# Kernel optimization log

Measured on AMD Instinct MI355X. Metric: run time of the kernel, lower is better.

Reference implementation:

```python
import jax, jax.numpy as jnp
import numpy as np


def _sig_gram(X, Y, n):
    """Signature-kernel gram matrix via the Goursat PDE recurrence.
    X: (A, M, D), Y: (B, N, D). Returns (A, B) of k(x_a, y_b).
    Recurrence: K[i+1,j+1] = K[i+1,j] + K[i,j+1] + K[i,j]*(inc_ij - 1).
    """
    f = 2 ** n
    # dyadic refinement: increments scaled by 1/2^n, each repeated 2^n times
    dX = jnp.repeat((X[:, 1:] - X[:, :-1]) / f, f, axis=1)  # (A, Mg-1, D)
    dY = jnp.repeat((Y[:, 1:] - Y[:, :-1]) / f, f, axis=1)  # (B, Ng-1, D)
    inc = jnp.einsum('aid,bjd->abij', dX, dY)               # (A, B, Mg-1, Ng-1)
    A, B, _, Ng1 = inc.shape
    ones_col = jnp.ones((A, B, 1), inc.dtype)

    def row_step(K_prev, inc_row):
        # K_prev: row i of the PDE grid, shape (A,B,Ng1+1); inc_row: (A,B,Ng1)
        diag = K_prev[..., :-1] * (inc_row - 1.0)  # K[i,j]*inc - K[i,j]
        up = K_prev[..., 1:]                        # K[i,j+1]

        def col_step(k_left, uv):
            u, d = uv
            k = k_left + u + d
            return k, k

        _, krow = jax.lax.scan(
            col_step,
            jnp.ones((A, B), inc.dtype),
            (jnp.moveaxis(up, -1, 0), jnp.moveaxis(diag, -1, 0)),
        )
        K_new = jnp.concatenate([ones_col, jnp.moveaxis(krow, 0, -1)], axis=-1)
        return K_new, None

    K0 = jnp.ones((A, B, Ng1 + 1), inc.dtype)  # boundary row K[0,:] = 1
    K_last, _ = jax.lax.scan(row_step, K0, jnp.moveaxis(inc, 2, 0))
    return K_last[..., -1]  # K[-1,-1] for every pair


def setup_inputs() -> dict:
    key = jax.random.key(0)
    kx, ky = jax.random.split(key)
    SCALE = 0.05  # keep kernel values in fp32 range (exponential growth)
    X = jax.random.normal(kx, (64, 128, 16), dtype=jnp.float32) * SCALE
    Y = jax.random.normal(ky, (64, 128, 16), dtype=jnp.float32) * SCALE
    return {"X": X, "Y": Y, "n": 0}


def reference(X, Y, n):
    k_xx = _sig_gram(X, X, n)
    k_yy = _sig_gram(Y, Y, n)
    k_xy = _sig_gram(X, Y, n)
    return jnp.mean(k_xx) + jnp.mean(k_yy) - 2.0 * jnp.mean(k_xy)
```

## Files before the change

kernel.cpp:

```cpp
#include <hip/hip_runtime.h>


#define XY_BLOCKS 1024
#define TRI_BLOCKS 544
#define NBLOCKS (XY_BLOCKS + 2 * TRI_BLOCKS)
#define DINC_PER 130048
#define WS_OUT_OFF (2 * DINC_PER)
#define NOUT (NBLOCKS * 4)

template <int C, int RM, int BM, bool BC>
__device__ __forceinline__ float dpp0(float x) {
    return __builtin_bit_cast(float, __builtin_amdgcn_update_dpp(
        0, __builtin_bit_cast(int, x), C, RM, BM, BC));
}

__device__ __forceinline__ float wave_scan_incl(float v) {
    v += dpp0<0x111, 0xf, 0xf, true>(v);
    v += dpp0<0x112, 0xf, 0xf, true>(v);
    v += dpp0<0x114, 0xf, 0xf, true>(v);
    v += dpp0<0x118, 0xf, 0xf, true>(v);
    v += dpp0<0x142, 0xa, 0xf, false>(v);
    v += dpp0<0x143, 0xc, 0xf, false>(v);
    return v;
}

__device__ __forceinline__ float wave_shr1(float x, float oldv) {
    return __builtin_bit_cast(float, __builtin_amdgcn_update_dpp(
        __builtin_bit_cast(int, oldv), __builtin_bit_cast(int, x),
        0x138, 0xf, 0xf, false));
}

__global__ __launch_bounds__(256) void sig_diff(
    const float* __restrict__ X, const float* __restrict__ Y,
    float* __restrict__ dInc)
{
    int i = blockIdx.x * 256 + threadIdx.x;
    if (i >= 65024) return;
    int which = (i >= 32512) ? 1 : 0;
    int j = i - which * 32512;
    int a = j / 508;
    int rq = j - a * 508;
    const float* S = which ? Y : X;
    const float4* p = (const float4*)(S + a * 2048) + rq;
    float4 v0 = p[0], v1 = p[4];
    float4 d;
    d.x = v1.x - v0.x; d.y = v1.y - v0.y;
    d.z = v1.z - v0.z; d.w = v1.w - v0.w;
    ((float4*)dInc)[i] = d;
}

__global__ __launch_bounds__(256) void sig_pde2(
    const float* __restrict__ dInc, float* __restrict__ outw)
{
    const int B = blockIdx.x;
    const int w = threadIdx.x >> 6, lane = threadIdx.x & 63;

    int g, a, b0;
    if (B < XY_BLOCKS) {
        g = 2; a = B >> 4; b0 = (B & 15) << 2;
    } else {
        int t = B - XY_BLOCKS; g = 0;
        if (t >= TRI_BLOCKS) { t -= TRI_BLOCKS; g = 1; }
        int aa = 0;
        for (;;) { int nb = (67 - aa) >> 2; if (t < nb) break; t -= nb; ++aa; }
        a = aa; b0 = aa + (t << 2);
    }
    const int b = b0 + w;
    const int slot = (B << 2) + w;
    if (g < 2 && b > 63) { if (lane == 0) outw[slot] = 0.0f; return; }

    const float* dXb = dInc;
    const float* dYb = dInc + DINC_PER;
    const float* dA = (g == 1) ? dYb : dXb;
    const float* dB = (g == 0) ? dXb : dYb;
    const float weight = (g == 2) ? (-2.0f / 4096.0f)
                                  : ((a == b ? 1.0f : 2.0f) / 4096.0f);

    float ya[16], yb_[16];
    {
        const float* Qb = dB + b * 2032;
        const int j0 = lane << 1;
        const int j1 = (j0 + 1 < 127) ? j0 + 1 : 126;
        const float4* A4 = (const float4*)(Qb + j0 * 16);
        const float4* B4 = (const float4*)(Qb + j1 * 16);
#pragma unroll
        for (int q = 0; q < 4; ++q) {
            float4 va = A4[q], vb = B4[q];
            ya[4*q+0] = va.x; ya[4*q+1] = va.y; ya[4*q+2] = va.z; ya[4*q+3] = va.w;
            yb_[4*q+0] = vb.x; yb_[4*q+1] = vb.y; yb_[4*q+2] = vb.z; yb_[4*q+3] = vb.w;
        }
    }

    const int abase = __builtin_amdgcn_readfirstlane(a * 2032);
    const float4* Ar = (const float4*)(dA + abase);

    float xr[16], xn[16];
#pragma unroll
    for (int q = 0; q < 4; ++q) {
        float4 v = Ar[q];
        xr[4*q+0] = v.x; xr[4*q+1] = v.y; xr[4*q+2] = v.z; xr[4*q+3] = v.w;
    }

    float g_lo = 1.0f, g_hi = 1.0f;
    const bool last = (lane == 63);

    for (int r = 0; r < 127; ++r) {
        const int rn = (r < 126) ? r + 1 : 126;
#pragma unroll
        for (int q = 0; q < 4; ++q) {
            float4 v = Ar[4 * rn + q];
            xn[4*q+0] = v.x; xn[4*q+1] = v.y; xn[4*q+2] = v.z; xn[4*q+3] = v.w;
        }
        float s0 = -0.5f, s1 = -0.5f, t0 = -0.5f, t1 = -0.5f;
#pragma unroll
        for (int d = 0; d < 16; d += 2) {
            s0 = fmaf(xr[d], ya[d], s0);    s1 = fmaf(xr[d+1], ya[d+1], s1);
            t0 = fmaf(xr[d], yb_[d], t0);   t1 = fmaf(xr[d+1], yb_[d+1], t1);
        }
        const float i0 = s0 + s1;
        const float i1 = t0 + t1;

        const float gl = wave_shr1(g_hi, 1.0f);
        const float c0 = fmaf(gl, i0, g_lo);
        const float c1 = last ? 0.0f : fmaf(g_lo, i1, g_hi);
        const float S = wave_scan_incl(c0 + c1);
        g_lo = (S - c1) + 1.0f;
        g_hi = S + 1.0f;
#pragma unroll
        for (int d = 0; d < 16; ++d) xr[d] = xn[d];
    }

    const float kab = __builtin_bit_cast(float,
        __builtin_amdgcn_readlane(__builtin_bit_cast(int, g_lo), 63));
    if (lane == 0) outw[slot] = weight * kab;
}

__global__ __launch_bounds__(256) void sig_reduce2(
    const float* __restrict__ v, float* __restrict__ out, int n)
{
    __shared__ float red[256];
    float s = 0.0f;
    for (int i = threadIdx.x; i < n; i += 256) s += v[i];
    red[threadIdx.x] = s;
    __syncthreads();
    for (int st = 128; st > 0; st >>= 1) {
        if (threadIdx.x < st) red[threadIdx.x] += red[threadIdx.x + st];
        __syncthreads();
    }
    if (threadIdx.x == 0) out[0] = red[0];
}

__global__ __launch_bounds__(64) void sig_pde_kernel(
    const float* __restrict__ X, const float* __restrict__ Y,
    float* __restrict__ ws)
{
    __shared__ float Xs[2048];
    const int T = blockIdx.x;
    const int g = T >> 12;
    const int t = T & 4095;
    const int a = t >> 6, b = t & 63;
    const int lane = threadIdx.x;
    if (g < 2 && a > b) { if (lane == 0) ws[T] = 0.0f; return; }
    const float* P = (g == 1) ? Y : X;
    const float* Q = (g == 0) ? X : Y;
    const float weight = (g == 2) ? (-2.0f / 4096.0f)
                                  : ((a == b ? 1.0f : 2.0f) / 4096.0f);
    {
        const float4* Pa = (const float4*)(P + a * 2048);
        float4* Xs4 = (float4*)Xs;
#pragma unroll
        for (int k = 0; k < 8; ++k) Xs4[lane + (k << 6)] = Pa[lane + (k << 6)];
    }
    __syncthreads();
    {
        float tmp[32];
#pragma unroll
        for (int k = 0; k < 32; ++k) {
            int idx = lane + (k << 6);
            tmp[k] = (idx < 2032) ? (Xs[idx + 16] - Xs[idx]) : 0.0f;
        }
        __syncthreads();
#pragma unroll
        for (int k = 0; k < 32; ++k) {
            int idx = lane + (k << 6);
            if (idx < 2032) Xs[idx] = tmp[k];
        }
    }
    __syncthreads();
    float y0[16], y1[16];
    {
        const float* Qb = Q + b * 2048;
        const int r0 = lane << 1;
        const int r2 = (r0 + 2 > 127) ? 127 : (r0 + 2);
        const float4* A4 = (const float4*)(Qb + r0 * 16);
        const float4* B4 = (const float4*)(Qb + (r0 + 1) * 16);
        const float4* C4 = (const float4*)(Qb + r2 * 16);
#pragma unroll
        for (int q = 0; q < 4; ++q) {
            float4 ra = A4[q], rb = B4[q], rc = C4[q];
            y0[4*q+0] = rb.x - ra.x;  y1[4*q+0] = rc.x - rb.x;
            y0[4*q+1] = rb.y - ra.y;  y1[4*q+1] = rc.y - rb.y;
            y0[4*q+2] = rb.z - ra.z;  y1[4*q+2] = rc.z - rb.z;
            y0[4*q+3] = rb.w - ra.w;  y1[4*q+3] = rc.w - rb.w;
        }
    }
    float g_lo = 1.0f, g_hi = 1.0f;
    const bool last = (lane == 63);
    for (int r = 0; r < 127; ++r) {
        const float* xrow = Xs + r * 16;
        float s0 = -0.5f, s1 = -0.5f, t0 = -0.5f, t1 = -0.5f;
#pragma unroll
        for (int d = 0; d < 16; d += 2) {
            s0 = fmaf(xrow[d], y0[d], s0);   s1 = fmaf(xrow[d+1], y0[d+1], s1);
            t0 = fmaf(xrow[d], y1[d], t0);   t1 = fmaf(xrow[d+1], y1[d+1], t1);
        }
        const float i0 = s0 + s1, i1 = t0 + t1;
        const float gl = wave_shr1(g_hi, 1.0f);
        const float c0 = fmaf(gl, i0, g_lo);
        const float c1 = last ? 0.0f : fmaf(g_lo, i1, g_hi);
        const float S = wave_scan_incl(c0 + c1);
        g_lo = (S - c1) + 1.0f;
        g_hi = S + 1.0f;
    }
    const float kab = __builtin_bit_cast(float,
        __builtin_amdgcn_readlane(__builtin_bit_cast(int, g_lo), 63));
    if (lane == 0) ws[T] = weight * kab;
}

extern "C" void kernel_launch(void* const* d_in, const int* in_sizes, int n_in,
                              void* d_out, int out_size, void* d_ws, size_t ws_size,
                              hipStream_t stream) {
    const float* X = (const float*)d_in[0];
    const float* Y = (const float*)d_in[1];
    float* out = (float*)d_out;
    float* ws  = (float*)d_ws;

    const size_t need = (size_t)(WS_OUT_OFF + NOUT) * sizeof(float);
    if (ws_size >= need) {
        sig_diff<<<254, 256, 0, stream>>>(X, Y, ws);
        sig_pde2<<<NBLOCKS, 256, 0, stream>>>(ws, ws + WS_OUT_OFF);
        sig_reduce2<<<1, 256, 0, stream>>>(ws + WS_OUT_OFF, out, NOUT);
    } else {
        sig_pde_kernel<<<12288, 64, 0, stream>>>(X, Y, ws);
        sig_reduce2<<<1, 256, 0, stream>>>(ws, out, 12288);
    }
}
```

Baseline: 149.4 us.

## Process two pairs per wave to interleave scans and fuse reduction via atomics

Each wave now computes the PDE for two (a,b) pairs that share the same x row, so the two independent DPP scan chains can interleave and hide each other's latency, and each loaded x row is reused twice. The triangular pair enumeration is changed to pack pairs in twos, which reduces wasted padded waves. The separate reduction kernel is removed: blocks sum their results in shared memory and atomically add into the output, which sig_diff zeroes first. This saves one kernel launch, but the fp32 atomic summation order becomes nondeterministic and each wave holds more registers.

```diff
diff --git a/kernel.cpp b/kernel.cpp
--- a/kernel.cpp
+++ b/kernel.cpp
@@ -1,12 +1,9 @@
 #include <hip/hip_runtime.h>
 
 
-#define XY_BLOCKS 1024
-#define TRI_BLOCKS 544
-#define NBLOCKS (XY_BLOCKS + 2 * TRI_BLOCKS)
 #define DINC_PER 130048
-#define WS_OUT_OFF (2 * DINC_PER)
-#define NOUT (NBLOCKS * 4)
+#define NDUO 4160
+#define NBLOCKS (NDUO / 4)
 
 template <int C, int RM, int BM, bool BC>
 __device__ __forceinline__ float dpp0(float x) {
@@ -30,10 +27,39 @@
         0x138, 0xf, 0xf, false));
 }
 
+__device__ __forceinline__ void pde_row(
+    const float* xr, const float* ya, const float* yb,
+    float& g_lo, float& g_hi, int lane)
+{
+    float s0 = -0.5f, s1 = -0.5f, t0 = -0.5f, t1 = -0.5f;
+#pragma unroll
+    for (int d = 0; d < 16; d += 2) {
+        s0 = fmaf(xr[d], ya[d], s0);    s1 = fmaf(xr[d+1], ya[d+1], s1);
+        t0 = fmaf(xr[d], yb[d], t0);    t1 = fmaf(xr[d+1], yb[d+1], t1);
+    }
+    const float i0 = s0 + s1;
+    const float i1 = t0 + t1;
+    const float gl = wave_shr1(g_hi, 1.0f);
+    const float c0 = fmaf(gl, i0, g_lo);
+    const float c1 = (lane == 63) ? 0.0f : fmaf(g_lo, i1, g_hi);
+    const float S = wave_scan_incl(c0 + c1);
+    g_lo = (S - c1) + 1.0f;
+    g_hi = S + 1.0f;
+}
+
+__device__ __forceinline__ void load_xrow(float* x, const float4* Ar, int r) {
+#pragma unroll
+    for (int q = 0; q < 4; ++q) {
+        float4 v = Ar[4 * r + q];
+        x[4*q+0] = v.x; x[4*q+1] = v.y; x[4*q+2] = v.z; x[4*q+3] = v.w;
+    }
+}
+
 __global__ __launch_bounds__(256) void sig_diff(
     const float* __restrict__ X, const float* __restrict__ Y,
-    float* __restrict__ dInc)
-{
+    float* __restrict__ dInc, float* __restrict__ outp)
+{
+    if (blockIdx.x == 0 && threadIdx.x == 0) outp[0] = 0.0f;
     int i = blockIdx.x * 256 + threadIdx.x;
     if (i >= 65024) return;
     int which = (i >= 32512) ? 1 : 0;
@@ -49,105 +75,79 @@
     ((float4*)dInc)[i] = d;
 }
 
-__global__ __launch_bounds__(256) void sig_pde2(
-    const float* __restrict__ dInc, float* __restrict__ outw)
-{
-    const int B = blockIdx.x;
-    const int w = threadIdx.x >> 6, lane = threadIdx.x & 63;
-
-    int g, a, b0;
-    if (B < XY_BLOCKS) {
-        g = 2; a = B >> 4; b0 = (B & 15) << 2;
+__global__ __launch_bounds__(256) void sig_pde3(
+    const float* __restrict__ dInc, float* __restrict__ outp)
+{
+    __shared__ float red[4];
+    const int wv = threadIdx.x >> 6, lane = threadIdx.x & 63;
+    const int T = (blockIdx.x << 2) + wv;
+
+    int g, a, b1, b2;
+    float w1, w2;
+    if (T < 2048) {
+        g = 2; a = T >> 5;
+        b1 = (T & 31) << 1; b2 = b1 + 1;
+        w1 = w2 = -2.0f / 4096.0f;
     } else {
-        int t = B - XY_BLOCKS; g = 0;
-        if (t >= TRI_BLOCKS) { t -= TRI_BLOCKS; g = 1; }
+        int t = T - 2048;
+        g = (t >= 1056) ? 1 : 0;
+        if (g) t -= 1056;
         int aa = 0;
-        for (;;) { int nb = (67 - aa) >> 2; if (t < nb) break; t -= nb; ++aa; }
-        a = aa; b0 = aa + (t << 2);
-    }
-    const int b = b0 + w;
-    const int slot = (B << 2) + w;
-    if (g < 2 && b > 63) { if (lane == 0) outw[slot] = 0.0f; return; }
-
-    const float* dXb = dInc;
-    const float* dYb = dInc + DINC_PER;
-    const float* dA = (g == 1) ? dYb : dXb;
-    const float* dB = (g == 0) ? dXb : dYb;
-    const float weight = (g == 2) ? (-2.0f / 4096.0f)
-                                  : ((a == b ? 1.0f : 2.0f) / 4096.0f);
-
-    float ya[16], yb_[16];
-    {
-        const float* Qb = dB + b * 2032;
+        for (;;) { int nd = (65 - aa) >> 1; if (t < nd) break; t -= nd; ++aa; }
+        a = aa; b1 = a + (t << 1); b2 = b1 + 1;
+        w1 = (b1 == a ? 1.0f : 2.0f) / 4096.0f;
+        w2 = (b2 <= 63) ? (2.0f / 4096.0f) : 0.0f;
+        if (b2 > 63) b2 = 63;
+    }
+
+    const float* dA = (g == 1) ? (dInc + DINC_PER) : dInc;
+    const float* dB = (g == 0) ? dInc : (dInc + DINC_PER);
+
+    float yaA[16], ybA[16], yaB[16], ybB[16];
+    {
         const int j0 = lane << 1;
         const int j1 = (j0 + 1 < 127) ? j0 + 1 : 126;
-        const float4* A4 = (const float4*)(Qb + j0 * 16);
-        const float4* B4 = (const float4*)(Qb + j1 * 16);
+        const float4* A4 = (const float4*)(dB + b1 * 2032 + j0 * 16);
+        const float4* B4 = (const float4*)(dB + b1 * 2032 + j1 * 16);
+        const float4* C4 = (const float4*)(dB + b2 * 2032 + j0 * 16);
+        const float4* D4 = (const float4*)(dB + b2 * 2032 + j1 * 16);
 #pragma unroll
         for (int q = 0; q < 4; ++q) {
-            float4 va = A4[q], vb = B4[q];
-            ya[4*q+0] = va.x; ya[4*q+1] = va.y; ya[4*q+2] = va.z; ya[4*q+3] = va.w;
-            yb_[4*q+0] = vb.x; yb_[4*q+1] = vb.y; yb_[4*q+2] = vb.z; yb_[4*q+3] = vb.w;
+            float4 va = A4[q], vb = B4[q], vc = C4[q], vd = D4[q];
+            yaA[4*q+0]=va.x; yaA[4*q+1]=va.y; yaA[4*q+2]=va.z; yaA[4*q+3]=va.w;
+            ybA[4*q+0]=vb.x; ybA[4*q+1]=vb.y; ybA[4*q+2]=vb.z; ybA[4*q+3]=vb.w;
+            yaB[4*q+0]=vc.x; yaB[4*q+1]=vc.y; yaB[4*q+2]=vc.z; yaB[4*q+3]=vc.w;
+            ybB[4*q+0]=vd.x; ybB[4*q+1]=vd.y; ybB[4*q+2]=vd.z; ybB[4*q+3]=vd.w;
         }
     }
 
     const int abase = __builtin_amdgcn_readfirstlane(a * 2032);
     const float4* Ar = (const float4*)(dA + abase);
 
-    float xr[16], xn[16];
-#pragma unroll
-    for (int q = 0; q < 4; ++q) {
-        float4 v = Ar[q];
-        xr[4*q+0] = v.x; xr[4*q+1] = v.y; xr[4*q+2] = v.z; xr[4*q+3] = v.w;
-    }
-
-    float g_lo = 1.0f, g_hi = 1.0f;
-    const bool last = (lane == 63);
-
-    for (int r = 0; r < 127; ++r) {
-        const int rn = (r < 126) ? r + 1 : 126;
-#pragma unroll
-        for (int q = 0; q < 4; ++q) {
-            float4 v = Ar[4 * rn + q];
-            xn[4*q+0] = v.x; xn[4*q+1] = v.y; xn[4*q+2] = v.z; xn[4*q+3] = v.w;
-        }
-        float s0 = -0.5f, s1 = -0.5f, t0 = -0.5f, t1 = -0.5f;
-#pragma unroll
-        for (int d = 0; d < 16; d += 2) {
-            s0 = fmaf(xr[d], ya[d], s0);    s1 = fmaf(xr[d+1], ya[d+1], s1);
-            t0 = fmaf(xr[d], yb_[d], t0);   t1 = fmaf(xr[d+1], yb_[d+1], t1);
-        }
-        const float i0 = s0 + s1;
-        const float i1 = t0 + t1;
-
-        const float gl = wave_shr1(g_hi, 1.0f);
-        const float c0 = fmaf(gl, i0, g_lo);
-        const float c1 = last ? 0.0f : fmaf(g_lo, i1, g_hi);
-        const float S = wave_scan_incl(c0 + c1);
-        g_lo = (S - c1) + 1.0f;
-        g_hi = S + 1.0f;
-#pragma unroll
-        for (int d = 0; d < 16; ++d) xr[d] = xn[d];
-    }
-
-    const float kab = __builtin_bit_cast(float,
-        __builtin_amdgcn_readlane(__builtin_bit_cast(int, g_lo), 63));
-    if (lane == 0) outw[slot] = weight * kab;
-}
-
-__global__ __launch_bounds__(256) void sig_reduce2(
-    const float* __restrict__ v, float* __restrict__ out, int n)
-{
-    __shared__ float red[256];
-    float s = 0.0f;
-    for (int i = threadIdx.x; i < n; i += 256) s += v[i];
-    red[threadIdx.x] = s;
-    __syncthreads();
-    for (int st = 128; st > 0; st >>= 1) {
-        if (threadIdx.x < st) red[threadIdx.x] += red[threadIdx.x + st];
-        __syncthreads();
-    }
-    if (threadIdx.x == 0) out[0] = red[0];
+    float xA[16], xB[16];
+    load_xrow(xA, Ar, 0);
+
+    float gl1 = 1.0f, gh1 = 1.0f, gl2 = 1.0f, gh2 = 1.0f;
+
+    for (int r = 0; r < 126; r += 2) {
+        load_xrow(xB, Ar, r + 1);
+        pde_row(xA, yaA, ybA, gl1, gh1, lane);
+        pde_row(xA, yaB, ybB, gl2, gh2, lane);
+        load_xrow(xA, Ar, r + 2);
+        pde_row(xB, yaA, ybA, gl1, gh1, lane);
+        pde_row(xB, yaB, ybB, gl2, gh2, lane);
+    }
+    pde_row(xA, yaA, ybA, gl1, gh1, lane);
+    pde_row(xA, yaB, ybB, gl2, gh2, lane);
+
+    const float k1 = __builtin_bit_cast(float,
+        __builtin_amdgcn_readlane(__builtin_bit_cast(int, gl1), 63));
+    const float k2 = __builtin_bit_cast(float,
+        __builtin_amdgcn_readlane(__builtin_bit_cast(int, gl2), 63));
+    if (lane == 0) red[wv] = fmaf(w1, k1, w2 * k2);
+    __syncthreads();
+    if (threadIdx.x == 0)
+        atomicAdd(outp, (red[0] + red[1]) + (red[2] + red[3]));
 }
 
 __global__ __launch_bounds__(64) void sig_pde_kernel(
@@ -205,26 +205,28 @@
         }
     }
     float g_lo = 1.0f, g_hi = 1.0f;
-    const bool last = (lane == 63);
     for (int r = 0; r < 127; ++r) {
         const float* xrow = Xs + r * 16;
-        float s0 = -0.5f, s1 = -0.5f, t0 = -0.5f, t1 = -0.5f;
-#pragma unroll
-        for (int d = 0; d < 16; d += 2) {
-            s0 = fmaf(xrow[d], y0[d], s0);   s1 = fmaf(xrow[d+1], y0[d+1], s1);
-            t0 = fmaf(xrow[d], y1[d], t0);   t1 = fmaf(xrow[d+1], y1[d+1], t1);
-        }
-        const float i0 = s0 + s1, i1 = t0 + t1;
-        const float gl = wave_shr1(g_hi, 1.0f);
-        const float c0 = fmaf(gl, i0, g_lo);
-        const float c1 = last ? 0.0f : fmaf(g_lo, i1, g_hi);
-        const float S = wave_scan_incl(c0 + c1);
-        g_lo = (S - c1) + 1.0f;
-        g_hi = S + 1.0f;
+        pde_row(xrow, y0, y1, g_lo, g_hi, lane);
     }
     const float kab = __builtin_bit_cast(float,
         __builtin_amdgcn_readlane(__builtin_bit_cast(int, g_lo), 63));
     if (lane == 0) ws[T] = weight * kab;
+}
+
+__global__ __launch_bounds__(256) void sig_reduce2(
+    const float* __restrict__ v, float* __restrict__ out, int n)
+{
+    __shared__ float red[256];
+    float s = 0.0f;
+    for (int i = threadIdx.x; i < n; i += 256) s += v[i];
+    red[threadIdx.x] = s;
+    __syncthreads();
+    for (int st = 128; st > 0; st >>= 1) {
+        if (threadIdx.x < st) red[threadIdx.x] += red[threadIdx.x + st];
+        __syncthreads();
+    }
+    if (threadIdx.x == 0) out[0] = red[0];
 }
 
 extern "C" void kernel_launch(void* const* d_in, const int* in_sizes, int n_in,
@@ -235,11 +237,9 @@
     float* out = (float*)d_out;
     float* ws  = (float*)d_ws;
 
-    const size_t need = (size_t)(WS_OUT_OFF + NOUT) * sizeof(float);
-    if (ws_size >= need) {
-        sig_diff<<<254, 256, 0, stream>>>(X, Y, ws);
-        sig_pde2<<<NBLOCKS, 256, 0, stream>>>(ws, ws + WS_OUT_OFF);
-        sig_reduce2<<<1, 256, 0, stream>>>(ws + WS_OUT_OFF, out, NOUT);
+    if (ws_size >= (size_t)(2 * DINC_PER) * sizeof(float)) {
+        sig_diff<<<254, 256, 0, stream>>>(X, Y, ws, out);
+        sig_pde3<<<NBLOCKS, 256, 0, stream>>>(ws, out);
     } else {
         sig_pde_kernel<<<12288, 64, 0, stream>>>(X, Y, ws);
         sig_reduce2<<<1, 256, 0, stream>>>(ws, out, 12288);
```

New measurement: 158.0 us. 5.7% more time.
